# Performance work log

Hardware: AMD Instinct MI355X
Metric: run time of the kernel (lower is better)

The kernel has to match this reference:

```python
import jax, jax.numpy as jnp
import numpy as np

N = 50000
IN_C = 128
HID = 128  # 2 * out_channels
OUT_C = 64
E = 800000


def setup_inputs() -> dict:
    key = jax.random.key(0)
    k1, k2, k3, k4, k5, k6 = jax.random.split(key, 6)
    x = jax.random.normal(k1, (N, IN_C), dtype=jnp.float32)
    edge_index = jax.random.randint(k2, (2, E), 0, N, dtype=jnp.int64)
    # Glorot init like PyG GCNConv
    W1 = jax.random.normal(k3, (IN_C, HID), dtype=jnp.float32) * np.sqrt(2.0 / (IN_C + HID))
    b1 = jnp.zeros((HID,), dtype=jnp.float32)
    W2 = jax.random.normal(k4, (HID, OUT_C), dtype=jnp.float32) * np.sqrt(2.0 / (HID + OUT_C))
    b2 = jnp.zeros((OUT_C,), dtype=jnp.float32)
    return {"x": x, "edge_index": edge_index, "W1": W1, "b1": b1, "W2": W2, "b2": b2}


def _gcn_norm(edge_index, num_nodes):
    # PyG gcn_norm with add_self_loops=True, edge_weight=1:
    # deg[i] = number of incoming edges to i (including self loop)
    # norm(e) = deg[src]^-0.5 * deg[dst]^-0.5
    loops = jnp.arange(num_nodes, dtype=edge_index.dtype)
    src = jnp.concatenate([edge_index[0], loops])
    dst = jnp.concatenate([edge_index[1], loops])
    deg = jax.ops.segment_sum(jnp.ones_like(dst, dtype=jnp.float32), dst,
                              num_segments=num_nodes)
    dinv = jnp.where(deg > 0, jax.lax.rsqrt(deg), 0.0)
    norm = dinv[src] * dinv[dst]
    return src, dst, norm


def _gcn_layer(x, W, b, src, dst, norm, num_nodes):
    h = x @ W                                    # [N, D_out] dense GEMM first (PyG order)
    msg = h[src] * norm[:, None]                 # gather + scale: [E+N, D_out]
    out = jax.ops.segment_sum(msg, dst, num_segments=num_nodes)  # scatter-add
    return out + b


def reference(x, edge_index, W1, b1, W2, b2):
    num_nodes = x.shape[0]
    # cached=True in the original: normalization computed once, reused by both convs
    src, dst, norm = _gcn_norm(edge_index, num_nodes)
    h = _gcn_layer(x, W1, b1, src, dst, norm, num_nodes)
    h = jax.nn.relu(h)
    out = _gcn_layer(h, W2, b2, src, dst, norm, num_nodes)
    return out
```

## Files before the change

kernel.cpp:

```cpp
#include <hip/hip_runtime.h>
#include <hip/hip_bf16.h>


typedef unsigned short ushort_t;
typedef __attribute__((ext_vector_type(8))) short bf16x8;
typedef __attribute__((ext_vector_type(4))) float f32x4;

__device__ __forceinline__ float blo(int v) {
    union { int i; float f; } u;
    u.i = v << 16;
    return u.f;
}

__device__ __forceinline__ float bhi(int v) {
    union { int i; float f; } u;
    u.i = v & 0xffff0000;
    return u.f;
}

__device__ __forceinline__ ushort_t f2bf(float f) {
    __hip_bfloat16 h = __float2bfloat16(f);
    return *reinterpret_cast<ushort_t*>(&h);
}

__device__ __forceinline__ int4 scale8(int4 v, float s) {
    int4 r;
    r.x = (int)(((unsigned)f2bf(bhi(v.x) * s) << 16) | f2bf(blo(v.x) * s));
    r.y = (int)(((unsigned)f2bf(bhi(v.y) * s) << 16) | f2bf(blo(v.y) * s));
    r.z = (int)(((unsigned)f2bf(bhi(v.z) * s) << 16) | f2bf(blo(v.z) * s));
    r.w = (int)(((unsigned)f2bf(bhi(v.w) * s) << 16) | f2bf(blo(v.w) * s));
    return r;
}

#define BSH 5
#define BNODES 32
#define BMAX 2048
#define CHUNK 4096
#define CAP 768
#define NPH 16
#define LDP 138


__global__ __launch_bounds__(256) void gemm1bin_k(const float* __restrict__ X,
                                                  const float* __restrict__ W,
                                                  ushort_t* __restrict__ H,
                                                  const int* __restrict__ src,
                                                  const int* __restrict__ dst,
                                                  int* __restrict__ bucket_cursor,
                                                  int* __restrict__ binned,
                                                  int n, int E, int nbin) {
    __shared__ __align__(16) char smem[52992];
    const int t = threadIdx.x;

    if ((int)blockIdx.x >= nbin) {
        ushort_t (*As)[LDP] = reinterpret_cast<ushort_t(*)[LDP]>(smem);
        ushort_t (*Bt)[LDP] = reinterpret_cast<ushort_t(*)[LDP]>(smem + 64 * LDP * 2);
        const int row0 = ((int)blockIdx.x - nbin) * 64;
#pragma unroll
        for (int rep = 0; rep < 8; rep++) {
            int idx = rep * 1024 + t * 4;
            int r = idx >> 7, c = idx & 127;
            int gr = row0 + r;
            float4 v = make_float4(0.f, 0.f, 0.f, 0.f);
            if (gr < n) v = *reinterpret_cast<const float4*>(X + (size_t)gr * 128 + c);
            As[r][c + 0] = f2bf(v.x); As[r][c + 1] = f2bf(v.y);
            As[r][c + 2] = f2bf(v.z); As[r][c + 3] = f2bf(v.w);
        }
#pragma unroll
        for (int rep = 0; rep < 16; rep++) {
            int idx = rep * 1024 + t * 4;
            int k = idx >> 7, nn = idx & 127;
            float4 v = *reinterpret_cast<const float4*>(W + k * 128 + nn);
            Bt[nn + 0][k] = f2bf(v.x); Bt[nn + 1][k] = f2bf(v.y);
            Bt[nn + 2][k] = f2bf(v.z); Bt[nn + 3][k] = f2bf(v.w);
        }
        __syncthreads();
        const int lane = t & 63;
        const int wave = t >> 6;
        const int l15 = lane & 15;
        const int koff = (lane >> 4) * 8;
        f32x4 acc[8] = {};
#pragma unroll
        for (int ks = 0; ks < 4; ks++) {
            int kb = ks * 32 + koff;
            bf16x8 a = *reinterpret_cast<const bf16x8*>(&As[wave * 16 + l15][kb]);
#pragma unroll
            for (int tc = 0; tc < 8; tc++) {
                bf16x8 b = *reinterpret_cast<const bf16x8*>(&Bt[tc * 16 + l15][kb]);
                acc[tc] = __builtin_amdgcn_mfma_f32_16x16x32_bf16(a, b, acc[tc], 0, 0, 0);
            }
        }
        const int rbase = row0 + wave * 16 + (lane >> 4) * 4;
#pragma unroll
        for (int reg = 0; reg < 4; reg++) {
            int gr = rbase + reg;
            if (gr < n) {
#pragma unroll
                for (int tc = 0; tc < 8; tc++)
                    H[(size_t)gr * 128 + tc * 16 + l15] = f2bf(acc[tc][reg]);
            }
        }
    } else {
        int* lcnt = (int*)smem;
        int* lbase = lcnt + BMAX;
        int* lcur = lbase + BMAX;
        const int nchunks = (E + CHUNK - 1) / CHUNK;
        for (int ch = (int)blockIdx.x; ch < nchunks; ch += nbin) {
            int base = ch * CHUNK;
            int cnt = min(CHUNK, E - base);
            for (int i = t; i < BMAX; i += 256) lcnt[i] = 0;
            __syncthreads();
            for (int k = t; k < cnt; k += 256)
                atomicAdd(&lcnt[dst[base + k] >> BSH], 1);
            __syncthreads();
            for (int i = t; i < BMAX; i += 256) {
                int c = lcnt[i];
                if (c) lbase[i] = atomicAdd(&bucket_cursor[i], c);
                lcur[i] = 0;
            }
            __syncthreads();
            for (int k = t; k < cnt; k += 256) {
                int d = dst[base + k];
                int b = d >> BSH;
                int r = atomicAdd(&lcur[b], 1);
                int pos = lbase[b] + r;
                if (pos < CAP)
                    binned[b * CAP + pos] = (src[base + k] << BSH) | (d & (BNODES - 1));
            }
            __syncthreads();
        }
    }
}

__global__ __launch_bounds__(256) void finalize_k(const int* __restrict__ binned,
                                                  const int* __restrict__ bucket_cursor,
                                                  float* __restrict__ dinv,
                                                  int2* __restrict__ row_range,
                                                  ushort_t* __restrict__ csr,
                                                  ushort_t* __restrict__ h1,
                                                  int N, int B) {
    __shared__ int cnt[BNODES][NPH];
    __shared__ int sc[BNODES];
    __shared__ float sdv[BNODES];
    int b = blockIdx.x;
    int tid = threadIdx.x;
    int node0 = b << BSH;
    int nn = min(BNODES, N - node0);
    int e0 = b * CAP;
    int e1 = e0 + min(bucket_cursor[b], CAP);
    const int phw = (N + NPH - 1) / NPH;

    for (int i = tid; i < BNODES * NPH; i += 256) ((int*)cnt)[i] = 0;
    __syncthreads();
    for (int k = e0 + tid; k < e1; k += 256) {
        int e = binned[k];
        int s = (int)((unsigned)e >> BSH);
        atomicAdd(&cnt[e & (BNODES - 1)][s / phw], 1);
    }
    __syncthreads();
    int deg = 0;
    int pre[NPH];
    if (tid < BNODES) {
#pragma unroll
        for (int p = 0; p < NPH; p++) { pre[p] = deg; deg += cnt[tid][p]; }
        sc[tid] = (tid < nn) ? deg : 0;
    }
    __syncthreads();
    for (int off = 1; off < BNODES; off <<= 1) {
        int t2 = 0;
        if (tid < BNODES && tid >= off) t2 = sc[tid - off];
        __syncthreads();
        if (tid < BNODES) sc[tid] += t2;
        __syncthreads();
    }
    if (tid < BNODES) {
        float dv = 0.f;
        if (tid < nn) {
            int ex = sc[tid] - deg;
            int g = node0 + tid;
            dv = rsqrtf((float)deg + 1.0f);
            dinv[g] = dv;
            row_range[g] = make_int2(e0 + ex, e0 + ex + deg);
#pragma unroll
            for (int p = 0; p < NPH; p++) cnt[tid][p] = ex + pre[p];
        }
        sdv[tid] = dv;
    }
    __syncthreads();
    for (int k = e0 + tid; k < e1; k += 256) {
        int e = binned[k];
        int s = (int)((unsigned)e >> BSH);
        int slot = atomicAdd(&cnt[e & (BNODES - 1)][s / phw], 1);
        csr[e0 + slot] = (ushort_t)s;
    }
    int4* h4 = reinterpret_cast<int4*>(h1);
    for (int idx = tid; idx < nn * 16; idx += 256) {
        int r = idx >> 4, c = idx & 15;
        size_t off = (size_t)(node0 + r) * 16 + c;
        h4[off] = scale8(h4[off], sdv[r]);
    }
}


__global__ __launch_bounds__(256) void gemm2_k(const ushort_t* __restrict__ X,
                                               const float* __restrict__ W,
                                               const float* __restrict__ dinv,
                                               ushort_t* __restrict__ H, int n) {
    __shared__ ushort_t As[64][LDP];
    __shared__ ushort_t Bt[64][LDP];
    const int t = threadIdx.x;
    const int row0 = blockIdx.x * 64;
#pragma unroll
    for (int rep = 0; rep < 8; rep++) {
        int idx = rep * 1024 + t * 4;
        int r = idx >> 7, c = idx & 127;
        int gr = row0 + r;
        ushort4 v = make_ushort4(0, 0, 0, 0);
        if (gr < n) v = *reinterpret_cast<const ushort4*>(X + (size_t)gr * 128 + c);
        As[r][c + 0] = v.x; As[r][c + 1] = v.y; As[r][c + 2] = v.z; As[r][c + 3] = v.w;
    }
#pragma unroll
    for (int rep = 0; rep < 8; rep++) {
        int idx = rep * 1024 + t * 4;
        int k = idx >> 6, nn = idx & 63;
        float4 v = *reinterpret_cast<const float4*>(W + k * 64 + nn);
        Bt[nn + 0][k] = f2bf(v.x); Bt[nn + 1][k] = f2bf(v.y);
        Bt[nn + 2][k] = f2bf(v.z); Bt[nn + 3][k] = f2bf(v.w);
    }
    __syncthreads();
    const int lane = t & 63;
    const int wave = t >> 6;
    const int l15 = lane & 15;
    const int koff = (lane >> 4) * 8;
    f32x4 acc[4] = {};
#pragma unroll
    for (int ks = 0; ks < 4; ks++) {
        int kb = ks * 32 + koff;
        bf16x8 a = *reinterpret_cast<const bf16x8*>(&As[wave * 16 + l15][kb]);
#pragma unroll
        for (int tc = 0; tc < 4; tc++) {
            bf16x8 b = *reinterpret_cast<const bf16x8*>(&Bt[tc * 16 + l15][kb]);
            acc[tc] = __builtin_amdgcn_mfma_f32_16x16x32_bf16(a, b, acc[tc], 0, 0, 0);
        }
    }
    const int rbase = row0 + wave * 16 + (lane >> 4) * 4;
#pragma unroll
    for (int reg = 0; reg < 4; reg++) {
        int gr = rbase + reg;
        if (gr < n) {
            float dv = dinv[gr];
#pragma unroll
            for (int tc = 0; tc < 4; tc++)
                H[(size_t)gr * 64 + tc * 16 + l15] = f2bf(acc[tc][reg] * dv);
        }
    }
}

#define FMA8(VV, WT)                                                    \
    a0 = fmaf(blo((VV).x), (WT), a0); a1 = fmaf(bhi((VV).x), (WT), a1); \
    a2 = fmaf(blo((VV).y), (WT), a2); a3 = fmaf(bhi((VV).y), (WT), a3); \
    a4 = fmaf(blo((VV).z), (WT), a4); a5 = fmaf(bhi((VV).z), (WT), a5); \
    a6 = fmaf(blo((VV).w), (WT), a6); a7 = fmaf(bhi((VV).w), (WT), a7);

#define ADD8(VV)                                  \
    a0 += blo((VV).x); a1 += bhi((VV).x);         \
    a2 += blo((VV).y); a3 += bhi((VV).y);         \
    a4 += blo((VV).z); a5 += bhi((VV).z);         \
    a6 += blo((VV).w); a7 += bhi((VV).w);


__global__ __launch_bounds__(256) void agg1_k(const ushort_t* __restrict__ h,
                                              const int2* __restrict__ row_range,
                                              const ushort_t* __restrict__ csr,
                                              const float* __restrict__ dinv,
                                              const float* __restrict__ bias,
                                              ushort_t* __restrict__ out, int n) {
    const int t = threadIdx.x;
    const int i = blockIdx.x * 16 + (t >> 4);
    if (i >= n) return;
    const int q = t & 15;
    const ushort_t* hq = h + 8 * q;
    float a0 = 0.f, a1 = 0.f, a2 = 0.f, a3 = 0.f;
    float a4 = 0.f, a5 = 0.f, a6 = 0.f, a7 = 0.f;
    const int2 rr = row_range[i];
    int j = rr.x;
    const int full_end = rr.x + ((rr.y - rr.x) & ~7);
    for (; j < full_end; j += 8) {
#pragma unroll
        for (int k = 0; k < 8; k++) {
            int s = (int)csr[j + k];
            int4 v = *reinterpret_cast<const int4*>(hq + (size_t)s * 128);
            ADD8(v);
        }
    }
    if (j < rr.y) {
        const int e = rr.y - 1;
#pragma unroll
        for (int k = 0; k < 8; k++) {
            int jk = min(j + k, e);
            int s = (int)csr[jk];
            float w = (j + k <= e) ? 1.f : 0.f;
            int4 v = *reinterpret_cast<const int4*>(hq + (size_t)s * 128);
            FMA8(v, w);
        }
    }
    const float di = dinv[i];
    int4 sv = *reinterpret_cast<const int4*>(hq + (size_t)i * 128);
    ADD8(sv);
    float4 b0 = *reinterpret_cast<const float4*>(bias + 8 * q);
    float4 b1v = *reinterpret_cast<const float4*>(bias + 8 * q + 4);
    int4 o;
    o.x = (int)(((unsigned)f2bf(fmaxf(fmaf(di, a1, b0.y), 0.f)) << 16) | f2bf(fmaxf(fmaf(di, a0, b0.x), 0.f)));
    o.y = (int)(((unsigned)f2bf(fmaxf(fmaf(di, a3, b0.w), 0.f)) << 16) | f2bf(fmaxf(fmaf(di, a2, b0.z), 0.f)));
    o.z = (int)(((unsigned)f2bf(fmaxf(fmaf(di, a5, b1v.y), 0.f)) << 16) | f2bf(fmaxf(fmaf(di, a4, b1v.x), 0.f)));
    o.w = (int)(((unsigned)f2bf(fmaxf(fmaf(di, a7, b1v.w), 0.f)) << 16) | f2bf(fmaxf(fmaf(di, a6, b1v.z), 0.f)));
    *reinterpret_cast<int4*>(out + (size_t)i * 128 + 8 * q) = o;
}


__global__ __launch_bounds__(256) void agg2_k(const ushort_t* __restrict__ h,
                                              const int2* __restrict__ row_range,
                                              const ushort_t* __restrict__ csr,
                                              const float* __restrict__ dinv,
                                              const float* __restrict__ bias,
                                              float* __restrict__ out, int n) {
    const int t = threadIdx.x;
    const int i = blockIdx.x * 32 + (t >> 3);
    if (i >= n) return;
    const int q = t & 7;
    const ushort_t* hq = h + 8 * q;
    float a0 = 0.f, a1 = 0.f, a2 = 0.f, a3 = 0.f;
    float a4 = 0.f, a5 = 0.f, a6 = 0.f, a7 = 0.f;
    const int2 rr = row_range[i];
    int j = rr.x;
    const int full_end = rr.x + ((rr.y - rr.x) & ~7);
    for (; j < full_end; j += 8) {
#pragma unroll
        for (int k = 0; k < 8; k++) {
            int s = (int)csr[j + k];
            int4 v = *reinterpret_cast<const int4*>(hq + (size_t)s * 64);
            ADD8(v);
        }
    }
    if (j < rr.y) {
        const int e = rr.y - 1;
#pragma unroll
        for (int k = 0; k < 8; k++) {
            int jk = min(j + k, e);
            int s = (int)csr[jk];
            float w = (j + k <= e) ? 1.f : 0.f;
            int4 v = *reinterpret_cast<const int4*>(hq + (size_t)s * 64);
            FMA8(v, w);
        }
    }
    int4 sv = *reinterpret_cast<const int4*>(hq + (size_t)i * 64);
    ADD8(sv);
    const float di = dinv[i];
    float4 b0 = *reinterpret_cast<const float4*>(bias + 8 * q);
    float4 b1v = *reinterpret_cast<const float4*>(bias + 8 * q + 4);
    float4 o0 = make_float4(fmaf(di, a0, b0.x), fmaf(di, a1, b0.y),
                            fmaf(di, a2, b0.z), fmaf(di, a3, b0.w));
    float4 o1 = make_float4(fmaf(di, a4, b1v.x), fmaf(di, a5, b1v.y),
                            fmaf(di, a6, b1v.z), fmaf(di, a7, b1v.w));
    *reinterpret_cast<float4*>(out + (size_t)i * 64 + 8 * q) = o0;
    *reinterpret_cast<float4*>(out + (size_t)i * 64 + 8 * q + 4) = o1;
}


extern "C" void kernel_launch(void* const* d_in, const int* in_sizes, int n_in,
                              void* d_out, int out_size, void* d_ws, size_t ws_size,
                              hipStream_t stream) {
    const float* x   = (const float*)d_in[0];
    const int*   ei  = (const int*)d_in[1];
    const float* W1  = (const float*)d_in[2];
    const float* b1  = (const float*)d_in[3];
    const float* W2  = (const float*)d_in[4];
    const float* b2  = (const float*)d_in[5];
    float* out = (float*)d_out;

    const int N = in_sizes[0] / 128;
    const int E = in_sizes[1] / 2;
    const int B = (N + BNODES - 1) >> BSH;
    const int* src = ei;
    const int* dst = ei + E;

    char* p = (char*)d_ws;
    auto alloc = [&](size_t bytes) {
        char* q = p;
        p += (bytes + 255) & ~(size_t)255;
        return (void*)q;
    };
    int*      bucket_cursor = (int*)alloc((size_t)BMAX * 4);
    float*    dinv          = (float*)alloc((size_t)N * 4);
    int2*     row_range     = (int2*)alloc((size_t)N * 8);
    int*      binned        = (int*)alloc((size_t)B * CAP * 4);
    ushort_t* csr           = (ushort_t*)alloc(((size_t)B * CAP + 32) * 2);
    ushort_t* h1            = (ushort_t*)alloc((size_t)N * 128 * 2);
    ushort_t* agg1          = (ushort_t*)alloc((size_t)N * 128 * 2);
    ushort_t* h2            = h1;

    const int nchunks = (E + CHUNK - 1) / CHUNK;
    const int G1 = (N + 63) / 64;

    (void)hipMemsetAsync(bucket_cursor, 0, (size_t)B * 4, stream);
    gemm1bin_k<<<nchunks + G1, 256, 0, stream>>>(x, W1, h1, src, dst,
                                                 bucket_cursor, binned, N, E, nchunks);
    finalize_k<<<B, 256, 0, stream>>>(binned, bucket_cursor, dinv, row_range, csr, h1, N, B);

    agg1_k<<<(N + 15) / 16, 256, 0, stream>>>(h1, row_range, csr, dinv, b1, agg1, N);

    gemm2_k<<<(N + 63) / 64, 256, 0, stream>>>(agg1, W2, dinv, h2, N);
    agg2_k<<<(N + 31) / 32, 256, 0, stream>>>(h2, row_range, csr, dinv, b2, out, N);
}
```

Measured before the change: 166.6 us.

## Fuse layer-1 aggregation with layer-2 GEMM in one kernel

Merges the first-layer aggregation kernel and the second GEMM into a single kernel. Each 16-row block aggregates neighbours, applies bias and ReLU, stores the bf16 result in shared memory, and multiplies it by W2 with MFMA before writing the scaled h2. This removes the round trip of the N×128 intermediate through global memory and one kernel launch. The cost is that every small block reloads and converts all of W2 into shared memory, and the extra shared memory may lower occupancy of the gather-bound aggregation.

```diff
diff --git a/kernel.cpp b/kernel.cpp
--- a/kernel.cpp
+++ b/kernel.cpp
@@ -201,61 +201,6 @@
     }
 }
 
-
-__global__ __launch_bounds__(256) void gemm2_k(const ushort_t* __restrict__ X,
-                                               const float* __restrict__ W,
-                                               const float* __restrict__ dinv,
-                                               ushort_t* __restrict__ H, int n) {
-    __shared__ ushort_t As[64][LDP];
-    __shared__ ushort_t Bt[64][LDP];
-    const int t = threadIdx.x;
-    const int row0 = blockIdx.x * 64;
-#pragma unroll
-    for (int rep = 0; rep < 8; rep++) {
-        int idx = rep * 1024 + t * 4;
-        int r = idx >> 7, c = idx & 127;
-        int gr = row0 + r;
-        ushort4 v = make_ushort4(0, 0, 0, 0);
-        if (gr < n) v = *reinterpret_cast<const ushort4*>(X + (size_t)gr * 128 + c);
-        As[r][c + 0] = v.x; As[r][c + 1] = v.y; As[r][c + 2] = v.z; As[r][c + 3] = v.w;
-    }
-#pragma unroll
-    for (int rep = 0; rep < 8; rep++) {
-        int idx = rep * 1024 + t * 4;
-        int k = idx >> 6, nn = idx & 63;
-        float4 v = *reinterpret_cast<const float4*>(W + k * 64 + nn);
-        Bt[nn + 0][k] = f2bf(v.x); Bt[nn + 1][k] = f2bf(v.y);
-        Bt[nn + 2][k] = f2bf(v.z); Bt[nn + 3][k] = f2bf(v.w);
-    }
-    __syncthreads();
-    const int lane = t & 63;
-    const int wave = t >> 6;
-    const int l15 = lane & 15;
-    const int koff = (lane >> 4) * 8;
-    f32x4 acc[4] = {};
-#pragma unroll
-    for (int ks = 0; ks < 4; ks++) {
-        int kb = ks * 32 + koff;
-        bf16x8 a = *reinterpret_cast<const bf16x8*>(&As[wave * 16 + l15][kb]);
-#pragma unroll
-        for (int tc = 0; tc < 4; tc++) {
-            bf16x8 b = *reinterpret_cast<const bf16x8*>(&Bt[tc * 16 + l15][kb]);
-            acc[tc] = __builtin_amdgcn_mfma_f32_16x16x32_bf16(a, b, acc[tc], 0, 0, 0);
-        }
-    }
-    const int rbase = row0 + wave * 16 + (lane >> 4) * 4;
-#pragma unroll
-    for (int reg = 0; reg < 4; reg++) {
-        int gr = rbase + reg;
-        if (gr < n) {
-            float dv = dinv[gr];
-#pragma unroll
-            for (int tc = 0; tc < 4; tc++)
-                H[(size_t)gr * 64 + tc * 16 + l15] = f2bf(acc[tc][reg] * dv);
-        }
-    }
-}
-
 #define FMA8(VV, WT)                                                    \
     a0 = fmaf(blo((VV).x), (WT), a0); a1 = fmaf(bhi((VV).x), (WT), a1); \
     a2 = fmaf(blo((VV).y), (WT), a2); a3 = fmaf(bhi((VV).y), (WT), a3); \
@@ -269,52 +214,90 @@
     a6 += blo((VV).w); a7 += bhi((VV).w);
 
 
-__global__ __launch_bounds__(256) void agg1_k(const ushort_t* __restrict__ h,
-                                              const int2* __restrict__ row_range,
-                                              const ushort_t* __restrict__ csr,
-                                              const float* __restrict__ dinv,
-                                              const float* __restrict__ bias,
-                                              ushort_t* __restrict__ out, int n) {
+__global__ __launch_bounds__(256) void agg1mm2_k(const ushort_t* __restrict__ h,
+                                                 const int2* __restrict__ row_range,
+                                                 const ushort_t* __restrict__ csr,
+                                                 const float* __restrict__ dinv,
+                                                 const float* __restrict__ b1,
+                                                 const float* __restrict__ W2,
+                                                 ushort_t* __restrict__ h2,
+                                                 int n) {
+    __shared__ ushort_t As[16][LDP];
+    __shared__ ushort_t Bt[64][LDP];
     const int t = threadIdx.x;
-    const int i = blockIdx.x * 16 + (t >> 4);
-    if (i >= n) return;
+    const int row0 = blockIdx.x * 16;
+
+#pragma unroll
+    for (int rep = 0; rep < 8; rep++) {
+        int idx = rep * 1024 + t * 4;
+        int k = idx >> 6, c = idx & 63;
+        float4 v = *reinterpret_cast<const float4*>(W2 + k * 64 + c);
+        Bt[c + 0][k] = f2bf(v.x); Bt[c + 1][k] = f2bf(v.y);
+        Bt[c + 2][k] = f2bf(v.z); Bt[c + 3][k] = f2bf(v.w);
+    }
+
+    const int i = row0 + (t >> 4);
     const int q = t & 15;
-    const ushort_t* hq = h + 8 * q;
-    float a0 = 0.f, a1 = 0.f, a2 = 0.f, a3 = 0.f;
-    float a4 = 0.f, a5 = 0.f, a6 = 0.f, a7 = 0.f;
-    const int2 rr = row_range[i];
-    int j = rr.x;
-    const int full_end = rr.x + ((rr.y - rr.x) & ~7);
-    for (; j < full_end; j += 8) {
-#pragma unroll
-        for (int k = 0; k < 8; k++) {
-            int s = (int)csr[j + k];
-            int4 v = *reinterpret_cast<const int4*>(hq + (size_t)s * 128);
-            ADD8(v);
-        }
-    }
-    if (j < rr.y) {
-        const int e = rr.y - 1;
-#pragma unroll
-        for (int k = 0; k < 8; k++) {
-            int jk = min(j + k, e);
-            int s = (int)csr[jk];
-            float w = (j + k <= e) ? 1.f : 0.f;
-            int4 v = *reinterpret_cast<const int4*>(hq + (size_t)s * 128);
-            FMA8(v, w);
-        }
-    }
-    const float di = dinv[i];
-    int4 sv = *reinterpret_cast<const int4*>(hq + (size_t)i * 128);
-    ADD8(sv);
-    float4 b0 = *reinterpret_cast<const float4*>(bias + 8 * q);
-    float4 b1v = *reinterpret_cast<const float4*>(bias + 8 * q + 4);
-    int4 o;
-    o.x = (int)(((unsigned)f2bf(fmaxf(fmaf(di, a1, b0.y), 0.f)) << 16) | f2bf(fmaxf(fmaf(di, a0, b0.x), 0.f)));
-    o.y = (int)(((unsigned)f2bf(fmaxf(fmaf(di, a3, b0.w), 0.f)) << 16) | f2bf(fmaxf(fmaf(di, a2, b0.z), 0.f)));
-    o.z = (int)(((unsigned)f2bf(fmaxf(fmaf(di, a5, b1v.y), 0.f)) << 16) | f2bf(fmaxf(fmaf(di, a4, b1v.x), 0.f)));
-    o.w = (int)(((unsigned)f2bf(fmaxf(fmaf(di, a7, b1v.w), 0.f)) << 16) | f2bf(fmaxf(fmaf(di, a6, b1v.z), 0.f)));
-    *reinterpret_cast<int4*>(out + (size_t)i * 128 + 8 * q) = o;
+    if (i < n) {
+        const ushort_t* hq = h + 8 * q;
+        float a0 = 0.f, a1 = 0.f, a2 = 0.f, a3 = 0.f;
+        float a4 = 0.f, a5 = 0.f, a6 = 0.f, a7 = 0.f;
+        const int2 rr = row_range[i];
+        int j = rr.x;
+        const int full_end = rr.x + ((rr.y - rr.x) & ~7);
+        for (; j < full_end; j += 8) {
+#pragma unroll
+            for (int k = 0; k < 8; k++) {
+                int s = (int)csr[j + k];
+                int4 v = *reinterpret_cast<const int4*>(hq + (size_t)s * 128);
+                ADD8(v);
+            }
+        }
+        if (j < rr.y) {
+            const int e = rr.y - 1;
+#pragma unroll
+            for (int k = 0; k < 8; k++) {
+                int jk = min(j + k, e);
+                int s = (int)csr[jk];
+                float w = (j + k <= e) ? 1.f : 0.f;
+                int4 v = *reinterpret_cast<const int4*>(hq + (size_t)s * 128);
+                FMA8(v, w);
+            }
+        }
+        const float di = dinv[i];
+        int4 sv = *reinterpret_cast<const int4*>(hq + (size_t)i * 128);
+        ADD8(sv);
+        float4 c0 = *reinterpret_cast<const float4*>(b1 + 8 * q);
+        float4 c1 = *reinterpret_cast<const float4*>(b1 + 8 * q + 4);
+        int4 o;
+        o.x = (int)(((unsigned)f2bf(fmaxf(fmaf(di, a1, c0.y), 0.f)) << 16) | f2bf(fmaxf(fmaf(di, a0, c0.x), 0.f)));
+        o.y = (int)(((unsigned)f2bf(fmaxf(fmaf(di, a3, c0.w), 0.f)) << 16) | f2bf(fmaxf(fmaf(di, a2, c0.z), 0.f)));
+        o.z = (int)(((unsigned)f2bf(fmaxf(fmaf(di, a5, c1.y), 0.f)) << 16) | f2bf(fmaxf(fmaf(di, a4, c1.x), 0.f)));
+        o.w = (int)(((unsigned)f2bf(fmaxf(fmaf(di, a7, c1.w), 0.f)) << 16) | f2bf(fmaxf(fmaf(di, a6, c1.z), 0.f)));
+        *reinterpret_cast<int4*>(&As[t >> 4][8 * q]) = o;
+    } else {
+        *reinterpret_cast<int4*>(&As[t >> 4][8 * q]) = make_int4(0, 0, 0, 0);
+    }
+    __syncthreads();
+
+    const int lane = t & 63;
+    const int wave = t >> 6;
+    const int l15 = lane & 15;
+    const int koff = (lane >> 4) * 8;
+    f32x4 acc = {};
+#pragma unroll
+    for (int ks = 0; ks < 4; ks++) {
+        int kb = ks * 32 + koff;
+        bf16x8 a = *reinterpret_cast<const bf16x8*>(&As[l15][kb]);
+        bf16x8 b = *reinterpret_cast<const bf16x8*>(&Bt[wave * 16 + l15][kb]);
+        acc = __builtin_amdgcn_mfma_f32_16x16x32_bf16(a, b, acc, 0, 0, 0);
+    }
+#pragma unroll
+    for (int reg = 0; reg < 4; reg++) {
+        int gr = row0 + (lane >> 4) * 4 + reg;
+        if (gr < n)
+            h2[(size_t)gr * 64 + wave * 16 + l15] = f2bf(acc[reg] * dinv[gr]);
+    }
 }
 
 
@@ -396,8 +379,7 @@
     int*      binned        = (int*)alloc((size_t)B * CAP * 4);
     ushort_t* csr           = (ushort_t*)alloc(((size_t)B * CAP + 32) * 2);
     ushort_t* h1            = (ushort_t*)alloc((size_t)N * 128 * 2);
-    ushort_t* agg1          = (ushort_t*)alloc((size_t)N * 128 * 2);
-    ushort_t* h2            = h1;
+    ushort_t* h2            = (ushort_t*)alloc((size_t)N * 64 * 2);
 
     const int nchunks = (E + CHUNK - 1) / CHUNK;
     const int G1 = (N + 63) / 64;
@@ -407,8 +389,7 @@
                                                  bucket_cursor, binned, N, E, nchunks);
     finalize_k<<<B, 256, 0, stream>>>(binned, bucket_cursor, dinv, row_range, csr, h1, N, B);
 
-    agg1_k<<<(N + 15) / 16, 256, 0, stream>>>(h1, row_range, csr, dinv, b1, agg1, N);
-
-    gemm2_k<<<(N + 63) / 64, 256, 0, stream>>>(agg1, W2, dinv, h2, N);
+    agg1mm2_k<<<(N + 15) / 16, 256, 0, stream>>>(h1, row_range, csr, dinv, b1, W2, h2, N);
+
     agg2_k<<<(N + 31) / 32, 256, 0, stream>>>(h2, row_range, csr, dinv, b2, out, N);
 }
```

After: 163.5 us, median of 2. No clear change (-1.8%).
